# Optimization experiments

Measured on AMD Instinct MI355X. Metric: run time of the kernel, lower is better.

The kernel has to match this reference:

```python
import jax, jax.numpy as jnp
import numpy as np

N = 50000      # nodes
E = 800000     # edges (avg degree 16)
SIZES = [128, 128, 128, 128, 64]
NUM_LAYERS = 4


def setup_inputs() -> dict:
    key = jax.random.key(0)
    ks = jax.random.split(key, 3 + 2 * NUM_LAYERS)
    inp = {
        "x": jax.random.normal(ks[0], (N, SIZES[0]), dtype=jnp.float32),
        "edge_index": jax.random.randint(ks[1], (2, E), 0, N, dtype=jnp.int64),
        "edge_weight": jax.random.uniform(ks[2], (E,), dtype=jnp.float32),
    }
    for i in range(NUM_LAYERS):
        fan_in = SIZES[i]
        inp[f"W{i}"] = (jax.random.normal(ks[3 + 2 * i], (SIZES[i], SIZES[i + 1]), dtype=jnp.float32)
                        / np.float32(np.sqrt(fan_in)))
        inp[f"b{i}"] = jnp.zeros((SIZES[i + 1],), dtype=jnp.float32)
    return inp


def gcn_conv(x, src, dst, ew, W, b, n):
    """PyG GCNConv with add_self_loops=True, normalize=True (eval mode).
    deg[i] = sum of incoming edge weights at i + 1 (self loop weight 1).
    norm(j->i) = deg[j]^-1/2 * w_ji * deg[i]^-1/2.
    Self loop contributes deg[i]^-1 * (xW)[i].
    """
    xw = x @ W                                                    # [n, out]
    deg = jax.ops.segment_sum(ew, dst, num_segments=n) + 1.0      # [n]
    dinv = jnp.where(deg > 0, jax.lax.rsqrt(deg), 0.0)            # deg^-1/2
    norm = dinv[src] * ew * dinv[dst]                             # [E]
    agg = jax.ops.segment_sum(xw[src] * norm[:, None], dst, num_segments=n)
    return agg + xw * (dinv * dinv)[:, None] + b


def reference(x, edge_index, edge_weight, W0, b0, W1, b1, W2, b2, W3, b3):
    # Dropout p=0.5 is identity in eval mode (training=False).
    src, dst = edge_index[0], edge_index[1]
    Ws = [W0, W1, W2, W3]
    bs = [b0, b1, b2, b3]
    for i in range(NUM_LAYERS):
        x = gcn_conv(x, src, dst, edge_weight, Ws[i], bs[i], N)
        if i < NUM_LAYERS - 1:
            x = jax.nn.relu(x)
    return x
```

## Files before the change

### kernel.cpp

```cpp
#include <hip/hip_runtime.h>
#include <hip/hip_fp16.h>


#define DEG_SCALE 4194304.0f
#define BCAP 5120
#define K1_EDGES 4096
#define ACT_LD 136

using f16x8 = __attribute__((ext_vector_type(8))) _Float16;
using f32x4 = __attribute__((ext_vector_type(4))) float;

__global__ void prep_kernel(const float* __restrict__ W0, const float* __restrict__ W1,
                            const float* __restrict__ W2, const float* __restrict__ W3,
                            __half* P0, __half* P1, __half* P2, __half* P3,
                            int* gCursor, int nBuckets) {
    int blk = blockIdx.x;
    if (blk == 28) {
        int t = threadIdx.x;
        if (t < nBuckets) gCursor[t] = t * BCAP;
        return;
    }
    int t = blk * 256 + threadIdx.x;
    const float* W;
    __half* P;
    int OUT;
    if (t < 2048)      { W = W0; P = P0; OUT = 128; }
    else if (t < 4096) { W = W1; P = P1; OUT = 128; t -= 2048; }
    else if (t < 6144) { W = W2; P = P2; OUT = 128; t -= 4096; }
    else               { W = W3; P = P3; OUT = 64;  t -= 6144; }
    int lane = t & 63, fi = t >> 6;
    int nt = fi >> 2, kc = fi & 3;
    int col = 16 * nt + (lane & 15);
    int k0  = 32 * kc + 8 * (lane >> 4);
    union { __half h[8]; uint4 u; } v;
#pragma unroll
    for (int j = 0; j < 8; j++) v.h[j] = __float2half_rn(W[(size_t)(k0 + j) * OUT + col]);
    *(uint4*)&P[((size_t)fi * 64 + lane) * 8] = v.u;
}

__global__ __launch_bounds__(256) void bucket_scatter_kernel(
        const int* __restrict__ src, const int* __restrict__ dst,
        const float* __restrict__ ew, int* gCursor,
        int2* __restrict__ bucketArr, int E, int nBuckets) {
    __shared__ int cnt[256];
    __shared__ int runBase[256];
    int tid = threadIdx.x;
    int e0 = blockIdx.x * K1_EDGES;
    int e1 = min(e0 + K1_EDGES, E);
    cnt[tid] = 0;
    __syncthreads();
    for (int e = e0 + tid; e < e1; e += 256)
        atomicAdd(&cnt[dst[e] >> 8], 1);
    __syncthreads();
    if (tid < nBuckets && cnt[tid] > 0)
        runBase[tid] = atomicAdd(&gCursor[tid], cnt[tid]);
    __syncthreads();
    cnt[tid] = 0;
    __syncthreads();
    for (int e = e0 + tid; e < e1; e += 256) {
        int d = dst[e];
        int b = d >> 8;
        int slot = runBase[b] + atomicAdd(&cnt[b], 1);
        if (slot < (b + 1) * BCAP)
            bucketArr[slot] = make_int2((src[e] & 0xFFFF) | (d << 16),
                                        __float_as_int(ew[e]));
    }
}

__global__ __launch_bounds__(256) void bucket_csr_kernel(
        const int2* __restrict__ bucketArr, const int* __restrict__ gCursor,
        int2* __restrict__ epack, int* __restrict__ row_ptr,
        float* __restrict__ dinv, float* __restrict__ dinv2,
        int N, int E, int nBuckets) {
    __shared__ int2 st[BCAP];
    __shared__ int cnt[256];
    __shared__ int scn[256];
    __shared__ int cur[256];
    __shared__ unsigned int dfix[256];
    __shared__ int cbase_sh;
    int b   = blockIdx.x;
    int tid = threadIdx.x;
    int node0 = b << 8;
    int nloc  = min(256, N - node0);
    int base  = b * BCAP;

    int sz = (tid < nBuckets) ? (gCursor[tid] - tid * BCAP) : 0;
    scn[tid] = sz;
    __syncthreads();
    for (int off = 1; off < 256; off <<= 1) {
        int u = (tid >= off) ? scn[tid - off] : 0;
        __syncthreads();
        scn[tid] += u;
        __syncthreads();
    }
    if (tid == b) cbase_sh = scn[tid] - sz;
    cnt[tid]  = 0;
    dfix[tid] = 0u;
    __syncthreads();
    int cbase = cbase_sh;
    int size  = gCursor[b] - base;

    for (int i = tid; i < size; i += 256) {
        int2 v = bucketArr[base + i];
        st[i] = v;
        int dl = (v.x >> 16) & 255;
        atomicAdd(&cnt[dl], 1);
        atomicAdd(&dfix[dl], (unsigned int)rintf(__int_as_float(v.y) * DEG_SCALE));
    }
    __syncthreads();

    if (tid < nloc) {
        float d = (float)dfix[tid] * (1.0f / DEG_SCALE) + 1.0f;
        float r = rsqrtf(d);
        dinv[node0 + tid]  = r;
        dinv2[node0 + tid] = 1.0f / d;
    }

    int val = cnt[tid];
    scn[tid] = val;
    __syncthreads();
    for (int off = 1; off < 256; off <<= 1) {
        int u = (tid >= off) ? scn[tid - off] : 0;
        __syncthreads();
        scn[tid] += u;
        __syncthreads();
    }
    int excl = scn[tid] - val;
    scn[tid] = excl;
    if (tid < nloc) row_ptr[node0 + tid] = cbase + excl;
    if (b == nBuckets - 1 && tid == 0) row_ptr[N] = E;
    cur[tid] = 0;
    __syncthreads();

    for (int i = tid; i < size; i += 256) {
        int2 v = st[i];
        int dl = (v.x >> 16) & 255;
        int p  = cbase + scn[dl] + atomicAdd(&cur[dl], 1);
        epack[p] = v;
    }
}

template <int OUT, bool AFP32>
__device__ __forceinline__ void gemm_body(const void* __restrict__ A,
                                          const __half* __restrict__ Wpack,
                                          __half* __restrict__ xw, int nrows, int bid) {
    constexpr int NT  = OUT / 16;
    constexpr int CPR = OUT / 8;
    __shared__ __half D[64 * OUT];
    int tid  = threadIdx.x;
    int wave = tid >> 6, lane = tid & 63;
    int r = lane & 15, g = lane >> 4;
    int row0 = bid * 64 + wave * 16;

    int arow = row0 + r;
    if (arow >= nrows) arow = nrows - 1;

    f16x8 a[4];
#pragma unroll
    for (int kc = 0; kc < 4; kc++) {
        if (AFP32) {
            const float* p = (const float*)A + (size_t)arow * 128 + kc * 32 + g * 8;
            float4 u = *(const float4*)p;
            float4 v = *(const float4*)(p + 4);
            a[kc][0] = (_Float16)u.x; a[kc][1] = (_Float16)u.y;
            a[kc][2] = (_Float16)u.z; a[kc][3] = (_Float16)u.w;
            a[kc][4] = (_Float16)v.x; a[kc][5] = (_Float16)v.y;
            a[kc][6] = (_Float16)v.z; a[kc][7] = (_Float16)v.w;
        } else {
            a[kc] = *(const f16x8*)((const __half*)A + (size_t)arow * 128 + kc * 32 + g * 8);
        }
    }

#pragma unroll
    for (int nt = 0; nt < NT; nt++) {
        const f16x8* Bp = (const f16x8*)(Wpack) + (size_t)nt * 4 * 64 + lane;
        f32x4 c = {0.f, 0.f, 0.f, 0.f};
        c = __builtin_amdgcn_mfma_f32_16x16x32_f16(a[0], Bp[0],   c, 0, 0, 0);
        c = __builtin_amdgcn_mfma_f32_16x16x32_f16(a[1], Bp[64],  c, 0, 0, 0);
        c = __builtin_amdgcn_mfma_f32_16x16x32_f16(a[2], Bp[128], c, 0, 0, 0);
        c = __builtin_amdgcn_mfma_f32_16x16x32_f16(a[3], Bp[192], c, 0, 0, 0);
        int col = 16 * nt + r;
#pragma unroll
        for (int j = 0; j < 4; j++) {
            int drow = wave * 16 + 4 * g + j;
            int ch   = (col >> 3) ^ (drow & (CPR - 1));
            D[drow * OUT + ch * 8 + (col & 7)] = __float2half_rn(c[j]);
        }
    }
    __syncthreads();
#pragma unroll
    for (int i = 0; i < 64 * CPR / 256; i++) {
        int idx  = tid + i * 256;
        int drow = idx / CPR;
        int ch   = idx % CPR;
        int gr   = bid * 64 + drow;
        if (gr < nrows) {
            f16x8 v = *(f16x8*)&D[drow * OUT + ((ch ^ (drow & (CPR - 1))) << 3)];
            *(f16x8*)&xw[(size_t)gr * OUT + ch * 8] = v;
        }
    }
}

__global__ __launch_bounds__(256) void norm_gemm0_kernel(
        int2* __restrict__ epack, const float* __restrict__ dinv, int E, int nbNorm,
        const float* __restrict__ x, const __half* __restrict__ Wpack,
        __half* __restrict__ xw, int nrows) {
    int blk = blockIdx.x;
    if (blk < nbNorm) {
        int i = blk * 256 + threadIdx.x;
        if (i < E) {
            int2 v = epack[i];
            int s = v.x & 0xFFFF;
            int d = (v.x >> 16) & 0xFFFF;
            float nm = dinv[s] * __int_as_float(v.y) * dinv[d];
            epack[i] = make_int2(s, __float_as_int(nm));
        }
        return;
    }
    gemm_body<128, true>(x, Wpack, xw, nrows, blk - nbNorm);
}

template <int OUT_NEXT>
__global__ __launch_bounds__(256) void gather_gemm_kernel(
        const __half* __restrict__ xwh,
        const int* __restrict__ rp,
        const int2* __restrict__ epack,
        const float* __restrict__ dinv2,
        const float* __restrict__ bias,
        const __half* __restrict__ Wpack,
        __half* __restrict__ xw_out,
        int n) {
    constexpr int NT  = OUT_NEXT / 16;
    constexpr int NTW = NT / 4;
    constexpr int CPR = OUT_NEXT / 8;
    __shared__ __half act[16 * ACT_LD];
    __shared__ __half D[16 * OUT_NEXT];
    int tid  = threadIdx.x;
    int wv   = tid >> 6, lane = tid & 63;
    int node0 = blockIdx.x * 16;

#pragma unroll
    for (int k = 0; k < 4; k++) {
        int lrow = wv * 4 + k;
        int node = node0 + lrow;
        if (node < n) {
            node = __builtin_amdgcn_readfirstlane(node);
            int e0 = rp[node], e1 = rp[node + 1];
            float ax = 0.f, ay = 0.f;
            int e = e0;
            for (; e + 8 <= e1; e += 8) {
                int2 v0 = epack[e + 0], v1 = epack[e + 1], v2 = epack[e + 2], v3 = epack[e + 3];
                int2 v4 = epack[e + 4], v5 = epack[e + 5], v6 = epack[e + 6], v7 = epack[e + 7];
                __half2 h0 = ((const __half2*)(xwh + (size_t)v0.x * 128))[lane];
                __half2 h1 = ((const __half2*)(xwh + (size_t)v1.x * 128))[lane];
                __half2 h2 = ((const __half2*)(xwh + (size_t)v2.x * 128))[lane];
                __half2 h3 = ((const __half2*)(xwh + (size_t)v3.x * 128))[lane];
                __half2 h4 = ((const __half2*)(xwh + (size_t)v4.x * 128))[lane];
                __half2 h5 = ((const __half2*)(xwh + (size_t)v5.x * 128))[lane];
                __half2 h6 = ((const __half2*)(xwh + (size_t)v6.x * 128))[lane];
                __half2 h7 = ((const __half2*)(xwh + (size_t)v7.x * 128))[lane];
                float w0 = __int_as_float(v0.y), w1 = __int_as_float(v1.y);
                float w2 = __int_as_float(v2.y), w3 = __int_as_float(v3.y);
                float w4 = __int_as_float(v4.y), w5 = __int_as_float(v5.y);
                float w6 = __int_as_float(v6.y), w7 = __int_as_float(v7.y);
                ax += __half2float(h0.x) * w0 + __half2float(h1.x) * w1
                    + __half2float(h2.x) * w2 + __half2float(h3.x) * w3
                    + __half2float(h4.x) * w4 + __half2float(h5.x) * w5
                    + __half2float(h6.x) * w6 + __half2float(h7.x) * w7;
                ay += __half2float(h0.y) * w0 + __half2float(h1.y) * w1
                    + __half2float(h2.y) * w2 + __half2float(h3.y) * w3
                    + __half2float(h4.y) * w4 + __half2float(h5.y) * w5
                    + __half2float(h6.y) * w6 + __half2float(h7.y) * w7;
            }
            for (; e + 2 <= e1; e += 2) {
                int2 v0 = epack[e + 0], v1 = epack[e + 1];
                __half2 h0 = ((const __half2*)(xwh + (size_t)v0.x * 128))[lane];
                __half2 h1 = ((const __half2*)(xwh + (size_t)v1.x * 128))[lane];
                float w0 = __int_as_float(v0.y), w1 = __int_as_float(v1.y);
                ax += __half2float(h0.x) * w0 + __half2float(h1.x) * w1;
                ay += __half2float(h0.y) * w0 + __half2float(h1.y) * w1;
            }
            for (; e < e1; e++) {
                int2 v = epack[e];
                __half2 h = ((const __half2*)(xwh + (size_t)v.x * 128))[lane];
                float w = __int_as_float(v.y);
                ax += __half2float(h.x) * w;
                ay += __half2float(h.y) * w;
            }
            float   d2 = dinv2[node];
            __half2 hs = ((const __half2*)(xwh + (size_t)node * 128))[lane];
            float2  bl = *(const float2*)&bias[lane * 2];
            float ox = fmaxf(ax + __half2float(hs.x) * d2 + bl.x, 0.f);
            float oy = fmaxf(ay + __half2float(hs.y) * d2 + bl.y, 0.f);
            __half2 ho;
            ho.x = __float2half_rn(ox);
            ho.y = __float2half_rn(oy);
            *(__half2*)&act[lrow * ACT_LD + lane * 2] = ho;
        }
    }
    __syncthreads();

    int r = lane & 15, g = lane >> 4;
    f16x8 a[4];
#pragma unroll
    for (int kc = 0; kc < 4; kc++)
        a[kc] = *(const f16x8*)&act[r * ACT_LD + kc * 32 + g * 8];

#pragma unroll
    for (int t = 0; t < NTW; t++) {
        int nt = wv * NTW + t;
        const f16x8* Bp = (const f16x8*)(Wpack) + (size_t)nt * 4 * 64 + lane;
        f32x4 c = {0.f, 0.f, 0.f, 0.f};
        c = __builtin_amdgcn_mfma_f32_16x16x32_f16(a[0], Bp[0],   c, 0, 0, 0);
        c = __builtin_amdgcn_mfma_f32_16x16x32_f16(a[1], Bp[64],  c, 0, 0, 0);
        c = __builtin_amdgcn_mfma_f32_16x16x32_f16(a[2], Bp[128], c, 0, 0, 0);
        c = __builtin_amdgcn_mfma_f32_16x16x32_f16(a[3], Bp[192], c, 0, 0, 0);
        int col = 16 * nt + r;
#pragma unroll
        for (int j = 0; j < 4; j++) {
            int drow = 4 * g + j;
            int ch   = (col >> 3) ^ (drow & (CPR - 1));
            D[drow * OUT_NEXT + ch * 8 + (col & 7)] = __float2half_rn(c[j]);
        }
    }
    __syncthreads();

    constexpr int CHUNKS = 16 * CPR;
    if (tid < CHUNKS) {
        int drow = tid / CPR;
        int ch   = tid % CPR;
        int gr   = node0 + drow;
        if (gr < n) {
            f16x8 v = *(f16x8*)&D[drow * OUT_NEXT + ((ch ^ (drow & (CPR - 1))) << 3)];
            *(f16x8*)&xw_out[(size_t)gr * OUT_NEXT + ch * 8] = v;
        }
    }
}

__global__ __launch_bounds__(256) void gather64h_kernel(const __half* __restrict__ xwh,
                                                        const int* __restrict__ rp,
                                                        const int2* __restrict__ epack,
                                                        const float* __restrict__ dinv2,
                                                        const float* __restrict__ bias,
                                                        float* __restrict__ out, int n) {
    int lane = threadIdx.x & 63;
    int node = (blockIdx.x * blockDim.x + threadIdx.x) >> 6;
    if (node >= n) return;
    node = __builtin_amdgcn_readfirstlane(node);
    int e0 = rp[node], e1 = rp[node + 1];
    float acc = 0.f;

    int e = e0;
    for (; e + 8 <= e1; e += 8) {
        int2 v0 = epack[e + 0], v1 = epack[e + 1], v2 = epack[e + 2], v3 = epack[e + 3];
        int2 v4 = epack[e + 4], v5 = epack[e + 5], v6 = epack[e + 6], v7 = epack[e + 7];
        float r0 = __half2float(xwh[(size_t)v0.x * 64 + lane]);
        float r1 = __half2float(xwh[(size_t)v1.x * 64 + lane]);
        float r2 = __half2float(xwh[(size_t)v2.x * 64 + lane]);
        float r3 = __half2float(xwh[(size_t)v3.x * 64 + lane]);
        float r4 = __half2float(xwh[(size_t)v4.x * 64 + lane]);
        float r5 = __half2float(xwh[(size_t)v5.x * 64 + lane]);
        float r6 = __half2float(xwh[(size_t)v6.x * 64 + lane]);
        float r7 = __half2float(xwh[(size_t)v7.x * 64 + lane]);
        acc += r0 * __int_as_float(v0.y) + r1 * __int_as_float(v1.y)
             + r2 * __int_as_float(v2.y) + r3 * __int_as_float(v3.y)
             + r4 * __int_as_float(v4.y) + r5 * __int_as_float(v5.y)
             + r6 * __int_as_float(v6.y) + r7 * __int_as_float(v7.y);
    }
    for (; e < e1; e++) {
        int2 v = epack[e];
        acc += __half2float(xwh[(size_t)v.x * 64 + lane]) * __int_as_float(v.y);
    }

    float self = __half2float(xwh[(size_t)node * 64 + lane]);
    out[(size_t)node * 64 + lane] = acc + self * dinv2[node] + bias[lane];
}

extern "C" void kernel_launch(void* const* d_in, const int* in_sizes, int n_in,
                              void* d_out, int out_size, void* d_ws, size_t ws_size,
                              hipStream_t stream) {
    const float* x  = (const float*)d_in[0];
    const int*   ei = (const int*)d_in[1];
    const float* ew = (const float*)d_in[2];
    const float* W[4] = {(const float*)d_in[3], (const float*)d_in[5],
                         (const float*)d_in[7], (const float*)d_in[9]};
    const float* b[4] = {(const float*)d_in[4], (const float*)d_in[6],
                         (const float*)d_in[8], (const float*)d_in[10]};
    const int N = in_sizes[0] / 128;
    const int E = in_sizes[2];
    const int* srcIdx = ei;
    const int* dstIdx = ei + E;
    float* out = (float*)d_out;

    const int nBuckets = (N + 255) / 256;

    char* p = (char*)d_ws;
    auto alloc = [&](size_t bytes) -> char* {
        char* q = p;
        p += (bytes + 255) / 256 * 256;
        return q;
    };
    float*  dinv      = (float*)alloc((size_t)N * 4);
    float*  dinv2     = (float*)alloc((size_t)N * 4);
    int*    row_ptr   = (int*)alloc((size_t)(N + 1) * 4);
    int*    gCursor   = (int*)alloc(256 * 4);
    int2*   bucketArr = (int2*)alloc((size_t)nBuckets * BCAP * 8);
    int2*   epack     = (int2*)alloc((size_t)E * 8);
    __half* xwA       = (__half*)alloc((size_t)N * 128 * 2);
    __half* xwB       = (__half*)alloc((size_t)N * 128 * 2);
    __half* Wp[4];
    Wp[0] = (__half*)alloc(128 * 128 * 2);
    Wp[1] = (__half*)alloc(128 * 128 * 2);
    Wp[2] = (__half*)alloc(128 * 128 * 2);
    Wp[3] = (__half*)alloc(128 * 64 * 2);

    const int k1_grid = (E + K1_EDGES - 1) / K1_EDGES;
    const int eb      = (E + 255) / 256;
    const int gemm_grid  = (N + 63) / 64;
    const int fused_grid = (N + 15) / 16;
    const int g64_grid   = (N + 3) / 4;

    prep_kernel<<<29, 256, 0, stream>>>(W[0], W[1], W[2], W[3],
                                        Wp[0], Wp[1], Wp[2], Wp[3],
                                        gCursor, nBuckets);
    bucket_scatter_kernel<<<k1_grid, 256, 0, stream>>>(srcIdx, dstIdx, ew, gCursor,
                                                       bucketArr, E, nBuckets);
    bucket_csr_kernel<<<nBuckets, 256, 0, stream>>>(bucketArr, gCursor, epack,
                                                    row_ptr, dinv, dinv2, N, E, nBuckets);
    norm_gemm0_kernel<<<eb + gemm_grid, 256, 0, stream>>>(epack, dinv, E, eb,
                                                          x, Wp[0], xwA, N);
    gather_gemm_kernel<128><<<fused_grid, 256, 0, stream>>>(
        xwA, row_ptr, epack, dinv2, b[0], Wp[1], xwB, N);
    gather_gemm_kernel<128><<<fused_grid, 256, 0, stream>>>(
        xwB, row_ptr, epack, dinv2, b[1], Wp[2], xwA, N);
    gather_gemm_kernel<64><<<fused_grid, 256, 0, stream>>>(
        xwA, row_ptr, epack, dinv2, b[2], Wp[3], xwB, N);
    gather64h_kernel<<<g64_grid, 256, 0, stream>>>(
        xwB, row_ptr, epack, dinv2, b[3], out, N);
}
```

Measured before the change: 182.7 us.

## Fold symmetric degree normalization into GEMM epilogues and drop per-edge norm pass

Instead of computing a per-edge norm dinv[s]*w*dinv[d] in a separate pass, the source-side dinv is applied as a row scale in the GEMM epilogue and the destination-side dinv after aggregation. Epack now stores raw edge weights, so the edge-normalization kernel and the dinv2 array go away. The gather-GEMM kernel is restructured so that each wave handles 16 nodes and a full output tile independently, which removes block-wide syncs. The cost is a wider block granularity and half-precision storage of the pre-scaled features. dinv is padded so the float4 loads past N stay in bounds.

```diff
diff --git a/kernel.cpp b/kernel.cpp
--- a/kernel.cpp
+++ b/kernel.cpp
@@ -70,8 +70,7 @@
 __global__ __launch_bounds__(256) void bucket_csr_kernel(
         const int2* __restrict__ bucketArr, const int* __restrict__ gCursor,
         int2* __restrict__ epack, int* __restrict__ row_ptr,
-        float* __restrict__ dinv, float* __restrict__ dinv2,
-        int N, int E, int nBuckets) {
+        float* __restrict__ dinv, int N, int E, int nBuckets) {
     __shared__ int2 st[BCAP];
     __shared__ int cnt[256];
     __shared__ int scn[256];
@@ -111,9 +110,7 @@
 
     if (tid < nloc) {
         float d = (float)dfix[tid] * (1.0f / DEG_SCALE) + 1.0f;
-        float r = rsqrtf(d);
-        dinv[node0 + tid]  = r;
-        dinv2[node0 + tid] = 1.0f / d;
+        dinv[node0 + tid] = rsqrtf(d);
     }
 
     int val = cnt[tid];
@@ -136,21 +133,20 @@
         int2 v = st[i];
         int dl = (v.x >> 16) & 255;
         int p  = cbase + scn[dl] + atomicAdd(&cur[dl], 1);
-        epack[p] = v;
-    }
-}
-
-template <int OUT, bool AFP32>
-__device__ __forceinline__ void gemm_body(const void* __restrict__ A,
-                                          const __half* __restrict__ Wpack,
-                                          __half* __restrict__ xw, int nrows, int bid) {
-    constexpr int NT  = OUT / 16;
-    constexpr int CPR = OUT / 8;
+        epack[p] = make_int2(v.x & 0xFFFF, v.y);
+    }
+}
+
+__global__ __launch_bounds__(256) void gemm0_kernel(const float* __restrict__ x,
+                                                    const __half* __restrict__ Wpack,
+                                                    const float* __restrict__ dinv,
+                                                    __half* __restrict__ xw, int nrows) {
+    constexpr int OUT = 128, NT = 8, CPR = 16;
     __shared__ __half D[64 * OUT];
     int tid  = threadIdx.x;
     int wave = tid >> 6, lane = tid & 63;
     int r = lane & 15, g = lane >> 4;
-    int row0 = bid * 64 + wave * 16;
+    int row0 = blockIdx.x * 64 + wave * 16;
 
     int arow = row0 + r;
     if (arow >= nrows) arow = nrows - 1;
@@ -158,18 +154,16 @@
     f16x8 a[4];
 #pragma unroll
     for (int kc = 0; kc < 4; kc++) {
-        if (AFP32) {
-            const float* p = (const float*)A + (size_t)arow * 128 + kc * 32 + g * 8;
-            float4 u = *(const float4*)p;
-            float4 v = *(const float4*)(p + 4);
-            a[kc][0] = (_Float16)u.x; a[kc][1] = (_Float16)u.y;
-            a[kc][2] = (_Float16)u.z; a[kc][3] = (_Float16)u.w;
-            a[kc][4] = (_Float16)v.x; a[kc][5] = (_Float16)v.y;
-            a[kc][6] = (_Float16)v.z; a[kc][7] = (_Float16)v.w;
-        } else {
-            a[kc] = *(const f16x8*)((const __half*)A + (size_t)arow * 128 + kc * 32 + g * 8);
-        }
-    }
+        const float* p = x + (size_t)arow * 128 + kc * 32 + g * 8;
+        float4 u = *(const float4*)p;
+        float4 v = *(const float4*)(p + 4);
+        a[kc][0] = (_Float16)u.x; a[kc][1] = (_Float16)u.y;
+        a[kc][2] = (_Float16)u.z; a[kc][3] = (_Float16)u.w;
+        a[kc][4] = (_Float16)v.x; a[kc][5] = (_Float16)v.y;
+        a[kc][6] = (_Float16)v.z; a[kc][7] = (_Float16)v.w;
+    }
+
+    float4 dv = *(const float4*)&dinv[row0 + 4 * g];
 
 #pragma unroll
     for (int nt = 0; nt < NT; nt++) {
@@ -179,6 +173,7 @@
         c = __builtin_amdgcn_mfma_f32_16x16x32_f16(a[1], Bp[64],  c, 0, 0, 0);
         c = __builtin_amdgcn_mfma_f32_16x16x32_f16(a[2], Bp[128], c, 0, 0, 0);
         c = __builtin_amdgcn_mfma_f32_16x16x32_f16(a[3], Bp[192], c, 0, 0, 0);
+        c[0] *= dv.x; c[1] *= dv.y; c[2] *= dv.z; c[3] *= dv.w;
         int col = 16 * nt + r;
 #pragma unroll
         for (int j = 0; j < 4; j++) {
@@ -189,35 +184,16 @@
     }
     __syncthreads();
 #pragma unroll
-    for (int i = 0; i < 64 * CPR / 256; i++) {
+    for (int i = 0; i < 4; i++) {
         int idx  = tid + i * 256;
         int drow = idx / CPR;
         int ch   = idx % CPR;
-        int gr   = bid * 64 + drow;
+        int gr   = blockIdx.x * 64 + drow;
         if (gr < nrows) {
             f16x8 v = *(f16x8*)&D[drow * OUT + ((ch ^ (drow & (CPR - 1))) << 3)];
             *(f16x8*)&xw[(size_t)gr * OUT + ch * 8] = v;
         }
     }
-}
-
-__global__ __launch_bounds__(256) void norm_gemm0_kernel(
-        int2* __restrict__ epack, const float* __restrict__ dinv, int E, int nbNorm,
-        const float* __restrict__ x, const __half* __restrict__ Wpack,
-        __half* __restrict__ xw, int nrows) {
-    int blk = blockIdx.x;
-    if (blk < nbNorm) {
-        int i = blk * 256 + threadIdx.x;
-        if (i < E) {
-            int2 v = epack[i];
-            int s = v.x & 0xFFFF;
-            int d = (v.x >> 16) & 0xFFFF;
-            float nm = dinv[s] * __int_as_float(v.y) * dinv[d];
-            epack[i] = make_int2(s, __float_as_int(nm));
-        }
-        return;
-    }
-    gemm_body<128, true>(x, Wpack, xw, nrows, blk - nbNorm);
 }
 
 template <int OUT_NEXT>
@@ -225,80 +201,75 @@
         const __half* __restrict__ xwh,
         const int* __restrict__ rp,
         const int2* __restrict__ epack,
-        const float* __restrict__ dinv2,
+        const float* __restrict__ dinv,
         const float* __restrict__ bias,
         const __half* __restrict__ Wpack,
         __half* __restrict__ xw_out,
         int n) {
     constexpr int NT  = OUT_NEXT / 16;
-    constexpr int NTW = NT / 4;
     constexpr int CPR = OUT_NEXT / 8;
-    __shared__ __half act[16 * ACT_LD];
-    __shared__ __half D[16 * OUT_NEXT];
+    __shared__ __half actAll[4 * 16 * ACT_LD];
     int tid  = threadIdx.x;
     int wv   = tid >> 6, lane = tid & 63;
-    int node0 = blockIdx.x * 16;
-
-#pragma unroll
-    for (int k = 0; k < 4; k++) {
-        int lrow = wv * 4 + k;
+    __half* act = &actAll[wv * 16 * ACT_LD];
+    int node0 = blockIdx.x * 64 + wv * 16;
+
+    for (int lrow = 0; lrow < 16; lrow++) {
         int node = node0 + lrow;
-        if (node < n) {
-            node = __builtin_amdgcn_readfirstlane(node);
-            int e0 = rp[node], e1 = rp[node + 1];
-            float ax = 0.f, ay = 0.f;
-            int e = e0;
-            for (; e + 8 <= e1; e += 8) {
-                int2 v0 = epack[e + 0], v1 = epack[e + 1], v2 = epack[e + 2], v3 = epack[e + 3];
-                int2 v4 = epack[e + 4], v5 = epack[e + 5], v6 = epack[e + 6], v7 = epack[e + 7];
-                __half2 h0 = ((const __half2*)(xwh + (size_t)v0.x * 128))[lane];
-                __half2 h1 = ((const __half2*)(xwh + (size_t)v1.x * 128))[lane];
-                __half2 h2 = ((const __half2*)(xwh + (size_t)v2.x * 128))[lane];
-                __half2 h3 = ((const __half2*)(xwh + (size_t)v3.x * 128))[lane];
-                __half2 h4 = ((const __half2*)(xwh + (size_t)v4.x * 128))[lane];
-                __half2 h5 = ((const __half2*)(xwh + (size_t)v5.x * 128))[lane];
-                __half2 h6 = ((const __half2*)(xwh + (size_t)v6.x * 128))[lane];
-                __half2 h7 = ((const __half2*)(xwh + (size_t)v7.x * 128))[lane];
-                float w0 = __int_as_float(v0.y), w1 = __int_as_float(v1.y);
-                float w2 = __int_as_float(v2.y), w3 = __int_as_float(v3.y);
-                float w4 = __int_as_float(v4.y), w5 = __int_as_float(v5.y);
-                float w6 = __int_as_float(v6.y), w7 = __int_as_float(v7.y);
-                ax += __half2float(h0.x) * w0 + __half2float(h1.x) * w1
-                    + __half2float(h2.x) * w2 + __half2float(h3.x) * w3
-                    + __half2float(h4.x) * w4 + __half2float(h5.x) * w5
-                    + __half2float(h6.x) * w6 + __half2float(h7.x) * w7;
-                ay += __half2float(h0.y) * w0 + __half2float(h1.y) * w1
-                    + __half2float(h2.y) * w2 + __half2float(h3.y) * w3
-                    + __half2float(h4.y) * w4 + __half2float(h5.y) * w5
-                    + __half2float(h6.y) * w6 + __half2float(h7.y) * w7;
-            }
-            for (; e + 2 <= e1; e += 2) {
-                int2 v0 = epack[e + 0], v1 = epack[e + 1];
-                __half2 h0 = ((const __half2*)(xwh + (size_t)v0.x * 128))[lane];
-                __half2 h1 = ((const __half2*)(xwh + (size_t)v1.x * 128))[lane];
-                float w0 = __int_as_float(v0.y), w1 = __int_as_float(v1.y);
-                ax += __half2float(h0.x) * w0 + __half2float(h1.x) * w1;
-                ay += __half2float(h0.y) * w0 + __half2float(h1.y) * w1;
-            }
-            for (; e < e1; e++) {
-                int2 v = epack[e];
-                __half2 h = ((const __half2*)(xwh + (size_t)v.x * 128))[lane];
-                float w = __int_as_float(v.y);
-                ax += __half2float(h.x) * w;
-                ay += __half2float(h.y) * w;
-            }
-            float   d2 = dinv2[node];
-            __half2 hs = ((const __half2*)(xwh + (size_t)node * 128))[lane];
-            float2  bl = *(const float2*)&bias[lane * 2];
-            float ox = fmaxf(ax + __half2float(hs.x) * d2 + bl.x, 0.f);
-            float oy = fmaxf(ay + __half2float(hs.y) * d2 + bl.y, 0.f);
-            __half2 ho;
-            ho.x = __float2half_rn(ox);
-            ho.y = __float2half_rn(oy);
-            *(__half2*)&act[lrow * ACT_LD + lane * 2] = ho;
-        }
-    }
-    __syncthreads();
+        if (node >= n) continue;
+        node = __builtin_amdgcn_readfirstlane(node);
+        int e0 = rp[node], e1 = rp[node + 1];
+        float ax = 0.f, ay = 0.f;
+        int e = e0;
+        for (; e + 8 <= e1; e += 8) {
+            int2 v0 = epack[e + 0], v1 = epack[e + 1], v2 = epack[e + 2], v3 = epack[e + 3];
+            int2 v4 = epack[e + 4], v5 = epack[e + 5], v6 = epack[e + 6], v7 = epack[e + 7];
+            __half2 h0 = ((const __half2*)(xwh + (size_t)v0.x * 128))[lane];
+            __half2 h1 = ((const __half2*)(xwh + (size_t)v1.x * 128))[lane];
+            __half2 h2 = ((const __half2*)(xwh + (size_t)v2.x * 128))[lane];
+            __half2 h3 = ((const __half2*)(xwh + (size_t)v3.x * 128))[lane];
+            __half2 h4 = ((const __half2*)(xwh + (size_t)v4.x * 128))[lane];
+            __half2 h5 = ((const __half2*)(xwh + (size_t)v5.x * 128))[lane];
+            __half2 h6 = ((const __half2*)(xwh + (size_t)v6.x * 128))[lane];
+            __half2 h7 = ((const __half2*)(xwh + (size_t)v7.x * 128))[lane];
+            float w0 = __int_as_float(v0.y), w1 = __int_as_float(v1.y);
+            float w2 = __int_as_float(v2.y), w3 = __int_as_float(v3.y);
+            float w4 = __int_as_float(v4.y), w5 = __int_as_float(v5.y);
+            float w6 = __int_as_float(v6.y), w7 = __int_as_float(v7.y);
+            ax += __half2float(h0.x) * w0 + __half2float(h1.x) * w1
+                + __half2float(h2.x) * w2 + __half2float(h3.x) * w3
+                + __half2float(h4.x) * w4 + __half2float(h5.x) * w5
+                + __half2float(h6.x) * w6 + __half2float(h7.x) * w7;
+            ay += __half2float(h0.y) * w0 + __half2float(h1.y) * w1
+                + __half2float(h2.y) * w2 + __half2float(h3.y) * w3
+                + __half2float(h4.y) * w4 + __half2float(h5.y) * w5
+                + __half2float(h6.y) * w6 + __half2float(h7.y) * w7;
+        }
+        for (; e + 2 <= e1; e += 2) {
+            int2 v0 = epack[e + 0], v1 = epack[e + 1];
+            __half2 h0 = ((const __half2*)(xwh + (size_t)v0.x * 128))[lane];
+            __half2 h1 = ((const __half2*)(xwh + (size_t)v1.x * 128))[lane];
+            float w0 = __int_as_float(v0.y), w1 = __int_as_float(v1.y);
+            ax += __half2float(h0.x) * w0 + __half2float(h1.x) * w1;
+            ay += __half2float(h0.y) * w0 + __half2float(h1.y) * w1;
+        }
+        for (; e < e1; e++) {
+            int2 v = epack[e];
+            __half2 h = ((const __half2*)(xwh + (size_t)v.x * 128))[lane];
+            float w = __int_as_float(v.y);
+            ax += __half2float(h.x) * w;
+            ay += __half2float(h.y) * w;
+        }
+        float   dvn = dinv[node];
+        __half2 hs  = ((const __half2*)(xwh + (size_t)node * 128))[lane];
+        float2  bl  = *(const float2*)&bias[lane * 2];
+        float ox = fmaxf(dvn * (ax + __half2float(hs.x)) + bl.x, 0.f);
+        float oy = fmaxf(dvn * (ay + __half2float(hs.y)) + bl.y, 0.f);
+        __half2 ho;
+        ho.x = __float2half_rn(ox);
+        ho.y = __float2half_rn(oy);
+        *(__half2*)&act[lrow * ACT_LD + lane * 2] = ho;
+    }
 
     int r = lane & 15, g = lane >> 4;
     f16x8 a[4];
@@ -306,32 +277,34 @@
     for (int kc = 0; kc < 4; kc++)
         a[kc] = *(const f16x8*)&act[r * ACT_LD + kc * 32 + g * 8];
 
-#pragma unroll
-    for (int t = 0; t < NTW; t++) {
-        int nt = wv * NTW + t;
+    float4 dvw = *(const float4*)&dinv[node0 + 4 * g];
+
+#pragma unroll
+    for (int nt = 0; nt < NT; nt++) {
         const f16x8* Bp = (const f16x8*)(Wpack) + (size_t)nt * 4 * 64 + lane;
         f32x4 c = {0.f, 0.f, 0.f, 0.f};
         c = __builtin_amdgcn_mfma_f32_16x16x32_f16(a[0], Bp[0],   c, 0, 0, 0);
         c = __builtin_amdgcn_mfma_f32_16x16x32_f16(a[1], Bp[64],  c, 0, 0, 0);
         c = __builtin_amdgcn_mfma_f32_16x16x32_f16(a[2], Bp[128], c, 0, 0, 0);
         c = __builtin_amdgcn_mfma_f32_16x16x32_f16(a[3], Bp[192], c, 0, 0, 0);
+        c[0] *= dvw.x; c[1] *= dvw.y; c[2] *= dvw.z; c[3] *= dvw.w;
         int col = 16 * nt + r;
 #pragma unroll
         for (int j = 0; j < 4; j++) {
             int drow = 4 * g + j;
             int ch   = (col >> 3) ^ (drow & (CPR - 1));
-            D[drow * OUT_NEXT + ch * 8 + (col & 7)] = __float2half_rn(c[j]);
-        }
-    }
-    __syncthreads();
-
-    constexpr int CHUNKS = 16 * CPR;
-    if (tid < CHUNKS) {
-        int drow = tid / CPR;
-        int ch   = tid % CPR;
+            act[drow * OUT_NEXT + ch * 8 + (col & 7)] = __float2half_rn(c[j]);
+        }
+    }
+
+#pragma unroll
+    for (int i = 0; i < 16 * CPR / 64; i++) {
+        int idx  = lane + i * 64;
+        int drow = idx / CPR;
+        int ch   = idx % CPR;
         int gr   = node0 + drow;
         if (gr < n) {
-            f16x8 v = *(f16x8*)&D[drow * OUT_NEXT + ((ch ^ (drow & (CPR - 1))) << 3)];
+            f16x8 v = *(f16x8*)&act[drow * OUT_NEXT + ((ch ^ (drow & (CPR - 1))) << 3)];
             *(f16x8*)&xw_out[(size_t)gr * OUT_NEXT + ch * 8] = v;
         }
     }
@@ -340,7 +313,7 @@
 __global__ __launch_bounds__(256) void gather64h_kernel(const __half* __restrict__ xwh,
                                                         const int* __restrict__ rp,
                                                         const int2* __restrict__ epack,
-                                                        const float* __restrict__ dinv2,
+                                                        const float* __restrict__ dinv,
                                                         const float* __restrict__ bias,
                                                         float* __restrict__ out, int n) {
     int lane = threadIdx.x & 63;
@@ -373,7 +346,7 @@
     }
 
     float self = __half2float(xwh[(size_t)node * 64 + lane]);
-    out[(size_t)node * 64 + lane] = acc + self * dinv2[node] + bias[lane];
+    out[(size_t)node * 64 + lane] = dinv[node] * (acc + self) + bias[lane];
 }
 
 extern "C" void kernel_launch(void* const* d_in, const int* in_sizes, int n_in,
@@ -400,8 +373,7 @@
         p += (bytes + 255) / 256 * 256;
         return q;
     };
-    float*  dinv      = (float*)alloc((size_t)N * 4);
-    float*  dinv2     = (float*)alloc((size_t)N * 4);
+    float*  dinv      = (float*)alloc((size_t)(N + 64) * 4);
     int*    row_ptr   = (int*)alloc((size_t)(N + 1) * 4);
     int*    gCursor   = (int*)alloc(256 * 4);
     int2*   bucketArr = (int2*)alloc((size_t)nBuckets * BCAP * 8);
@@ -414,10 +386,9 @@
     Wp[2] = (__half*)alloc(128 * 128 * 2);
     Wp[3] = (__half*)alloc(128 * 64 * 2);
 
-    const int k1_grid = (E + K1_EDGES - 1) / K1_EDGES;
-    const int eb      = (E + 255) / 256;
+    const int k1_grid    = (E + K1_EDGES - 1) / K1_EDGES;
     const int gemm_grid  = (N + 63) / 64;
-    const int fused_grid = (N + 15) / 16;
+    const int fused_grid = (N + 63) / 64;
     const int g64_grid   = (N + 3) / 4;
 
     prep_kernel<<<29, 256, 0, stream>>>(W[0], W[1], W[2], W[3],
@@ -426,15 +397,14 @@
     bucket_scatter_kernel<<<k1_grid, 256, 0, stream>>>(srcIdx, dstIdx, ew, gCursor,
                                                        bucketArr, E, nBuckets);
     bucket_csr_kernel<<<nBuckets, 256, 0, stream>>>(bucketArr, gCursor, epack,
-                                                    row_ptr, dinv, dinv2, N, E, nBuckets);
-    norm_gemm0_kernel<<<eb + gemm_grid, 256, 0, stream>>>(epack, dinv, E, eb,
-                                                          x, Wp[0], xwA, N);
+                                                    row_ptr, dinv, N, E, nBuckets);
+    gemm0_kernel<<<gemm_grid, 256, 0, stream>>>(x, Wp[0], dinv, xwA, N);
     gather_gemm_kernel<128><<<fused_grid, 256, 0, stream>>>(
-        xwA, row_ptr, epack, dinv2, b[0], Wp[1], xwB, N);
+        xwA, row_ptr, epack, dinv, b[0], Wp[1], xwB, N);
     gather_gemm_kernel<128><<<fused_grid, 256, 0, stream>>>(
-        xwB, row_ptr, epack, dinv2, b[1], Wp[2], xwA, N);
+        xwB, row_ptr, epack, dinv, b[1], Wp[2], xwA, N);
     gather_gemm_kernel<64><<<fused_grid, 256, 0, stream>>>(
-        xwA, row_ptr, epack, dinv2, b[2], Wp[3], xwB, N);
+        xwA, row_ptr, epack, dinv, b[2], Wp[3], xwB, N);
     gather64h_kernel<<<g64_grid, 256, 0, stream>>>(
-        xwB, row_ptr, epack, dinv2, b[3], out, N);
-}
+        xwB, row_ptr, epack, dinv, b[3], out, N);
+}
```

Result: slower. 226.5 us (+24.0%).
